# Optimization experiments

Measured on AMD Instinct MI355X. Metric: run time of the kernel, lower is better.

Reference implementation:

```python
import jax, jax.numpy as jnp
import numpy as np

N_NODES = 100000


def setup_inputs() -> dict:
    key = jax.random.key(0)
    k1, k2, k3, k4 = jax.random.split(key, 4)
    node_features = jax.random.normal(k1, (N_NODES, 128), dtype=jnp.float32)
    edge_index = jax.random.randint(k2, (2, 600000), 0, N_NODES, dtype=jnp.int64)
    weight = jax.random.normal(k3, (256, 256), dtype=jnp.float32) * (1.0 / np.sqrt(256.0))
    bias = jax.random.normal(k4, (1, 256), dtype=jnp.float32) * (1.0 / np.sqrt(256.0))
    return {"node_features": node_features, "edge_index": edge_index, "weight": weight, "bias": bias}


def reference(node_features, edge_index, weight, bias):
    N = node_features.shape[0]
    row, col = edge_index[0], edge_index[1]
    # remove self loops: mask edges where row == col
    valid = (row != col).astype(node_features.dtype)  # [E]
    gathered = node_features[col] * valid[:, None]  # [E, d]
    sums = jax.ops.segment_sum(gathered, row, num_segments=N)  # [N, d]
    counts = jax.ops.segment_sum(valid, row, num_segments=N)  # [N]
    # scatter_mean: divide by count, clamped to >= 1
    out = sums / jnp.maximum(counts, 1.0)[:, None]
    output = jnp.concatenate((out, node_features), axis=1)  # [N, 2d]
    output = output @ weight + bias  # [N, out_features]
    # F.normalize(p=2, dim=-1, eps=1e-12)
    norm = jnp.linalg.norm(output, axis=-1, keepdims=True)
    output = output / jnp.maximum(norm, 1e-12)
    return output
```

## Files before the change

### kernel.cpp

```cpp
#include <hip/hip_runtime.h>
#include <hip/hip_bf16.h>

#define N_NODES 100000
#define N_EDGES 600000
#define DFEAT 128
#define DOUT 256
#define BSTRIDE 32
#define BCAP 31
#define CVT_BLOCKS (N_NODES * DFEAT / 4 / 256)
#define WT_BLOCKS 32

typedef __attribute__((ext_vector_type(8))) short bf16x8;
typedef __attribute__((ext_vector_type(4))) float floatx4;

__device__ __forceinline__ short f32_to_bfbits(float f) {
    __hip_bfloat16 h = __float2bfloat16(f);
    return *reinterpret_cast<short*>(&h);
}
__device__ __forceinline__ float bfbits_to_f32(short s) {
    return __uint_as_float(((unsigned)(unsigned short)s) << 16);
}

__global__ void __launch_bounds__(256)
prep_kernel(const float* __restrict__ nf, __hip_bfloat16* __restrict__ nfb,
            const float* __restrict__ w, short* __restrict__ wtf,
            int* __restrict__ ebuf) {
    int b = blockIdx.x;
    int tid = threadIdx.x;
    if (b < CVT_BLOCKS) {
        int i = b * 256 + tid;
        float4 v = reinterpret_cast<const float4*>(nf)[i];
        short4 o;
        o.x = f32_to_bfbits(v.x); o.y = f32_to_bfbits(v.y);
        o.z = f32_to_bfbits(v.z); o.w = f32_to_bfbits(v.w);
        reinterpret_cast<short4*>(nfb)[i] = o;
        if (i < N_NODES) ebuf[i * BSTRIDE] = 0;
    } else {
        int e = (b - CVT_BLOCKS) * 256 + tid;
        int lane = e & 63;
        int kt = (e >> 6) & 7;
        int cb = e >> 9;
        int m = lane & 15;
        int q = lane >> 4;
        int n = cb * 16 + m;
        int k0 = kt * 32 + q * 8;
        bf16x8 t;
        #pragma unroll
        for (int j = 0; j < 8; ++j)
            t[j] = f32_to_bfbits(w[(size_t)(k0 + j) * DOUT + n]);
        reinterpret_cast<bf16x8*>(wtf)[e] = t;
    }
}

__global__ void __launch_bounds__(256)
fill_bucket_kernel(const int* __restrict__ ei, int* __restrict__ ebuf) {
    int e = blockIdx.x * blockDim.x + threadIdx.x;
    if (e >= N_EDGES) return;
    int r = ei[e];
    int c = ei[N_EDGES + e];
    if (r == c) return;
    int pos = atomicAdd(&ebuf[r * BSTRIDE], 1);
    if (pos < BCAP) ebuf[r * BSTRIDE + 1 + pos] = c;
}

__global__ void __launch_bounds__(256)
agg_kernel(const __hip_bfloat16* __restrict__ nfb,
           const int* __restrict__ ebuf,
           __hip_bfloat16* __restrict__ agg) {
    int gt  = blockIdx.x * 256 + threadIdx.x;
    int row = gt >> 3;
    int h   = gt & 7;

    const int* bp = ebuf + (size_t)row * BSTRIDE;
    int4 h0 = *reinterpret_cast<const int4*>(bp);
    int4 h1 = *reinterpret_cast<const int4*>(bp + 4);
    int4 h2 = *reinterpret_cast<const int4*>(bp + 8);
    int d = h0.x < BCAP ? h0.x : BCAP;

    const __hip_bfloat16* nbase = nfb + h * 16;

    float facc[2][8];
    #pragma unroll
    for (int half = 0; half < 2; ++half)
        #pragma unroll
        for (int i = 0; i < 8; ++i) facc[half][i] = 0.f;

    int idx[11] = {h0.y, h0.z, h0.w, h1.x, h1.y, h1.z, h1.w,
                   h2.x, h2.y, h2.z, h2.w};
    #pragma unroll
    for (int j = 0; j < 11; ++j) {
        int   cj = j < d ? idx[j] : row;
        float wj = j < d ? 1.0f : 0.0f;
        const __hip_bfloat16* p = nbase + (size_t)cj * DFEAT;
        bf16x8 v0 = *reinterpret_cast<const bf16x8*>(p);
        bf16x8 v1 = *reinterpret_cast<const bf16x8*>(p + 8);
        #pragma unroll
        for (int i = 0; i < 8; ++i) {
            facc[0][i] = fmaf(bfbits_to_f32(v0[i]), wj, facc[0][i]);
            facc[1][i] = fmaf(bfbits_to_f32(v1[i]), wj, facc[1][i]);
        }
    }
    if (d > 11) {
        for (int j = 11; j < d; ++j) {
            int cj = bp[1 + j];
            const __hip_bfloat16* p = nbase + (size_t)cj * DFEAT;
            bf16x8 v0 = *reinterpret_cast<const bf16x8*>(p);
            bf16x8 v1 = *reinterpret_cast<const bf16x8*>(p + 8);
            #pragma unroll
            for (int i = 0; i < 8; ++i) {
                facc[0][i] += bfbits_to_f32(v0[i]);
                facc[1][i] += bfbits_to_f32(v1[i]);
            }
        }
    }

    float invc = 1.0f / fmaxf((float)d, 1.0f);
    __hip_bfloat16* orow = agg + (size_t)row * DFEAT + h * 16;
    #pragma unroll
    for (int half = 0; half < 2; ++half) {
        bf16x8 a;
        #pragma unroll
        for (int i = 0; i < 8; ++i) a[i] = f32_to_bfbits(facc[half][i] * invc);
        *reinterpret_cast<bf16x8*>(orow + half * 8) = a;
    }
}

__device__ __forceinline__ void stage_half(const int4* __restrict__ wtf4, int half,
                                           int4* sh4, int wave, int lane) {
    const int4* src = wtf4 + half * 4096;
    #pragma unroll
    for (int it = 0; it < 8; ++it) {
        int idx = it * 512 + wave * 64;
        __builtin_amdgcn_global_load_lds(
            (const __attribute__((address_space(1))) void*)(src + idx + lane),
            (__attribute__((address_space(3))) void*)(sh4 + idx),
            16, 0, 0);
    }
}

__global__ void __launch_bounds__(512, 4)
gemm_kernel(const __hip_bfloat16* __restrict__ nfb,
            const __hip_bfloat16* __restrict__ agg,
            const short* __restrict__ wtf,
            const float* __restrict__ bias,
            float* __restrict__ out) {
    __shared__ int4 sh4[4096];
    const short* shs = reinterpret_cast<const short*>(sh4);
    const int4* wtf4 = reinterpret_cast<const int4*>(wtf);

    int tid  = threadIdx.x;
    int wave = tid >> 6;
    int lane = tid & 63;
    int m    = lane & 15;
    int q    = lane >> 4;

    stage_half(wtf4, 0, sh4, wave, lane);

    int rowBase = blockIdx.x * 128 + wave * 16;
    int arow = rowBase + m;
    if (arow >= N_NODES) arow = N_NODES - 1;

    bf16x8 afrag[8];
    const __hip_bfloat16* grow = agg + (size_t)arow * DFEAT + q * 8;
    const __hip_bfloat16* srow = nfb + (size_t)arow * DFEAT + q * 8;
    #pragma unroll
    for (int kt = 0; kt < 4; ++kt) {
        afrag[kt]     = *reinterpret_cast<const bf16x8*>(grow + kt * 32);
        afrag[4 + kt] = *reinterpret_cast<const bf16x8*>(srow + kt * 32);
    }

    __syncthreads();

    floatx4 acc[16];
    #pragma unroll
    for (int cb = 0; cb < 16; ++cb) acc[cb] = (floatx4){0.f, 0.f, 0.f, 0.f};

    #pragma unroll
    for (int kt = 0; kt < 8; ++kt) {
        bf16x8 a = afrag[kt];
        #pragma unroll
        for (int cbl = 0; cbl < 8; ++cbl) {
            bf16x8 b = *reinterpret_cast<const bf16x8*>(
                shs + ((size_t)(cbl * 8 + kt) * 64 + lane) * 8);
            acc[cbl] = __builtin_amdgcn_mfma_f32_16x16x32_bf16(a, b, acc[cbl], 0, 0, 0);
        }
    }

    __syncthreads();
    stage_half(wtf4, 1, sh4, wave, lane);
    __syncthreads();

    #pragma unroll
    for (int kt = 0; kt < 8; ++kt) {
        bf16x8 a = afrag[kt];
        #pragma unroll
        for (int cbl = 0; cbl < 8; ++cbl) {
            bf16x8 b = *reinterpret_cast<const bf16x8*>(
                shs + ((size_t)(cbl * 8 + kt) * 64 + lane) * 8);
            acc[8 + cbl] = __builtin_amdgcn_mfma_f32_16x16x32_bf16(a, b, acc[8 + cbl], 0, 0, 0);
        }
    }

    float ss[4] = {0.f, 0.f, 0.f, 0.f};
    #pragma unroll
    for (int cb = 0; cb < 16; ++cb) {
        float bv = bias[cb * 16 + m];
        #pragma unroll
        for (int rg = 0; rg < 4; ++rg) {
            float v = acc[cb][rg] + bv;
            acc[cb][rg] = v;
            ss[rg] += v * v;
        }
    }
    #pragma unroll
    for (int s = 1; s < 16; s <<= 1) {
        #pragma unroll
        for (int rg = 0; rg < 4; ++rg) ss[rg] += __shfl_xor(ss[rg], s, 64);
    }
    #pragma unroll
    for (int rg = 0; rg < 4; ++rg) {
        int r = rowBase + q * 4 + rg;
        if (r >= N_NODES) continue;
        float inv = 1.0f / fmaxf(sqrtf(ss[rg]), 1e-12f);
        size_t base = (size_t)r * DOUT + m;
        #pragma unroll
        for (int cb = 0; cb < 16; ++cb)
            __builtin_nontemporal_store(acc[cb][rg] * inv, &out[base + cb * 16]);
    }
}

extern "C" void kernel_launch(void* const* d_in, const int* in_sizes, int n_in,
                              void* d_out, int out_size, void* d_ws, size_t ws_size,
                              hipStream_t stream) {
    const float* nf   = (const float*)d_in[0];
    const int*   ei   = (const int*)d_in[1];
    const float* w    = (const float*)d_in[2];
    const float* bias = (const float*)d_in[3];
    float* out = (float*)d_out;

    __hip_bfloat16* nfb = (__hip_bfloat16*)d_ws;
    __hip_bfloat16* agg = nfb + (size_t)N_NODES * DFEAT;
    int* ebuf = (int*)(agg + (size_t)N_NODES * DFEAT);
    short* wtf = (short*)(ebuf + (size_t)N_NODES * BSTRIDE);

    prep_kernel<<<CVT_BLOCKS + WT_BLOCKS, 256, 0, stream>>>(nf, nfb, w, wtf, ebuf);

    int eb = (N_EDGES + 255) / 256;
    fill_bucket_kernel<<<eb, 256, 0, stream>>>(ei, ebuf);

    int ab = N_NODES / 32;
    agg_kernel<<<ab, 256, 0, stream>>>(nfb, ebuf, agg);

    int gb = (N_NODES + 127) / 128;
    gemm_kernel<<<gb, 512, 0, stream>>>(nfb, agg, wtf, bias, out);
}
```

Before: 250.6 us.

## Split GEMM output columns across wave pairs and stage full weight in LDS

The GEMM kernel now launches 1024 threads per block, with two waves per 16-row tile, each computing half of the 256 output columns. The whole bf16 weight (128 KB) is staged into LDS at once, which removes the second staging pass and its barriers. The two waves combine their partial L2-norm sums through a small shared array. Accumulator registers per wave are halved, but each wave now loads the A fragment redundantly, LDS use per block doubles (limiting blocks per CU), and output stores are no longer nontemporal.

New measurement: 252.0 us. About the same (+0.6%).

```diff
diff --git a/kernel.cpp b/kernel.cpp
--- a/kernel.cpp
+++ b/kernel.cpp
@@ -125,26 +125,14 @@
     }
 }
 
-__device__ __forceinline__ void stage_half(const int4* __restrict__ wtf4, int half,
-                                           int4* sh4, int wave, int lane) {
-    const int4* src = wtf4 + half * 4096;
-    #pragma unroll
-    for (int it = 0; it < 8; ++it) {
-        int idx = it * 512 + wave * 64;
-        __builtin_amdgcn_global_load_lds(
-            (const __attribute__((address_space(1))) void*)(src + idx + lane),
-            (__attribute__((address_space(3))) void*)(sh4 + idx),
-            16, 0, 0);
-    }
-}
-
-__global__ void __launch_bounds__(512, 4)
+__global__ void __launch_bounds__(1024, 4)
 gemm_kernel(const __hip_bfloat16* __restrict__ nfb,
             const __hip_bfloat16* __restrict__ agg,
             const short* __restrict__ wtf,
             const float* __restrict__ bias,
             float* __restrict__ out) {
-    __shared__ int4 sh4[4096];
+    __shared__ int4 sh4[8192];
+    __shared__ float sred[8][2][16];
     const short* shs = reinterpret_cast<const short*>(sh4);
     const int4* wtf4 = reinterpret_cast<const int4*>(wtf);
 
@@ -153,10 +141,19 @@
     int lane = tid & 63;
     int m    = lane & 15;
     int q    = lane >> 4;
-
-    stage_half(wtf4, 0, sh4, wave, lane);
-
-    int rowBase = blockIdx.x * 128 + wave * 16;
+    int t    = wave >> 1;
+    int h    = wave & 1;
+
+    #pragma unroll
+    for (int it = 0; it < 8; ++it) {
+        int idx = it * 1024 + wave * 64;
+        __builtin_amdgcn_global_load_lds(
+            (const __attribute__((address_space(1))) void*)(wtf4 + idx + lane),
+            (__attribute__((address_space(3))) void*)(sh4 + idx),
+            16, 0, 0);
+    }
+
+    int rowBase = blockIdx.x * 128 + t * 16;
     int arow = rowBase + m;
     if (arow >= N_NODES) arow = N_NODES - 1;
 
@@ -171,61 +168,54 @@
 
     __syncthreads();
 
-    floatx4 acc[16];
-    #pragma unroll
-    for (int cb = 0; cb < 16; ++cb) acc[cb] = (floatx4){0.f, 0.f, 0.f, 0.f};
+    floatx4 acc[8];
+    #pragma unroll
+    for (int cbl = 0; cbl < 8; ++cbl) acc[cbl] = (floatx4){0.f, 0.f, 0.f, 0.f};
 
     #pragma unroll
     for (int kt = 0; kt < 8; ++kt) {
         bf16x8 a = afrag[kt];
         #pragma unroll
         for (int cbl = 0; cbl < 8; ++cbl) {
+            int cb = h * 8 + cbl;
             bf16x8 b = *reinterpret_cast<const bf16x8*>(
-                shs + ((size_t)(cbl * 8 + kt) * 64 + lane) * 8);
+                shs + ((size_t)(cb * 8 + kt) * 64 + lane) * 8);
             acc[cbl] = __builtin_amdgcn_mfma_f32_16x16x32_bf16(a, b, acc[cbl], 0, 0, 0);
         }
     }
 
+    float ss[4] = {0.f, 0.f, 0.f, 0.f};
+    #pragma unroll
+    for (int cbl = 0; cbl < 8; ++cbl) {
+        float bv = bias[(h * 8 + cbl) * 16 + m];
+        #pragma unroll
+        for (int rg = 0; rg < 4; ++rg) {
+            float v = acc[cbl][rg] + bv;
+            acc[cbl][rg] = v;
+            ss[rg] += v * v;
+        }
+    }
+    #pragma unroll
+    for (int s = 1; s < 16; s <<= 1) {
+        #pragma unroll
+        for (int rg = 0; rg < 4; ++rg) ss[rg] += __shfl_xor(ss[rg], s, 64);
+    }
+    if (m == 0) {
+        #pragma unroll
+        for (int rg = 0; rg < 4; ++rg) sred[t][h][q * 4 + rg] = ss[rg];
+    }
     __syncthreads();
-    stage_half(wtf4, 1, sh4, wave, lane);
-    __syncthreads();
-
-    #pragma unroll
-    for (int kt = 0; kt < 8; ++kt) {
-        bf16x8 a = afrag[kt];
-        #pragma unroll
-        for (int cbl = 0; cbl < 8; ++cbl) {
-            bf16x8 b = *reinterpret_cast<const bf16x8*>(
-                shs + ((size_t)(cbl * 8 + kt) * 64 + lane) * 8);
-            acc[8 + cbl] = __builtin_amdgcn_mfma_f32_16x16x32_bf16(a, b, acc[8 + cbl], 0, 0, 0);
-        }
-    }
-
-    float ss[4] = {0.f, 0.f, 0.f, 0.f};
-    #pragma unroll
-    for (int cb = 0; cb < 16; ++cb) {
-        float bv = bias[cb * 16 + m];
-        #pragma unroll
-        for (int rg = 0; rg < 4; ++rg) {
-            float v = acc[cb][rg] + bv;
-            acc[cb][rg] = v;
-            ss[rg] += v * v;
-        }
-    }
-    #pragma unroll
-    for (int s = 1; s < 16; s <<= 1) {
-        #pragma unroll
-        for (int rg = 0; rg < 4; ++rg) ss[rg] += __shfl_xor(ss[rg], s, 64);
-    }
+
     #pragma unroll
     for (int rg = 0; rg < 4; ++rg) {
         int r = rowBase + q * 4 + rg;
         if (r >= N_NODES) continue;
-        float inv = 1.0f / fmaxf(sqrtf(ss[rg]), 1e-12f);
+        float tot = ss[rg] + sred[t][h ^ 1][q * 4 + rg];
+        float inv = 1.0f / fmaxf(sqrtf(tot), 1e-12f);
         size_t base = (size_t)r * DOUT + m;
         #pragma unroll
-        for (int cb = 0; cb < 16; ++cb)
-            __builtin_nontemporal_store(acc[cb][rg] * inv, &out[base + cb * 16]);
+        for (int cbl = 0; cbl < 8; ++cbl)
+            out[base + (h * 8 + cbl) * 16] = acc[cbl][rg] * inv;
     }
 }
 
@@ -252,5 +242,5 @@
     agg_kernel<<<ab, 256, 0, stream>>>(nfb, ebuf, agg);
 
     int gb = (N_NODES + 127) / 128;
-    gemm_kernel<<<gb, 512, 0, stream>>>(nfb, agg, wtf, bias, out);
-}
+    gemm_kernel<<<gb, 1024, 0, stream>>>(nfb, agg, wtf, bias, out);
+}
```
